# Optimization experiments

Measured on AMD Instinct MI355X. Metric: run time of the kernel, lower is better.

The kernel has to match this reference:

```python
import jax, jax.numpy as jnp
import numpy as np

VOCAB, E, H, L, B, OUT = 50000, 300, 300, 75, 2048, 5

def setup_inputs() -> dict:
    key = jax.random.key(0)
    ks = jax.random.split(key, 12)
    s_e = 1.0 / np.sqrt(E)
    s_h = 1.0 / np.sqrt(H)
    return {
        "input_sequences": jax.random.randint(ks[0], (B, L), 0, VOCAB),
        "emb": jax.random.normal(ks[1], (VOCAB, E), jnp.float32) * 0.1,
        "W_ih": jax.random.normal(ks[2], (3 * H, E), jnp.float32) * s_e,
        "W_hh": jax.random.normal(ks[3], (3 * H, H), jnp.float32) * s_h,
        "b_ih": jax.random.normal(ks[4], (3 * H,), jnp.float32) * s_h,
        "b_hh": jax.random.normal(ks[5], (3 * H,), jnp.float32) * s_h,
        "wCo_w": jax.random.normal(ks[6], (3 * H,), jnp.float32) * (1.0 / np.sqrt(3 * H)),
        "wCo_b": jax.random.normal(ks[7], (1,), jnp.float32) * 0.02,
        "Wmy_w": jax.random.normal(ks[8], (L,), jnp.float32) * (1.0 / np.sqrt(L)),
        "Wmy_b": jax.random.normal(ks[9], (1,), jnp.float32) * 0.02,
        "logits_w": jax.random.normal(ks[10], (OUT, H), jnp.float32) * s_h,
        "logits_b": jax.random.normal(ks[11], (OUT,), jnp.float32) * 0.02,
    }

def _gru(x_tm, W_ih, W_hh, b_ih, b_hh):
    # x_tm: (L, B, E) time-major. PyTorch GRU cell math.
    gx_all = jnp.einsum("lbe,ge->lbg", x_tm, W_ih) + b_ih  # (L, B, 3H)
    h0 = jnp.zeros((x_tm.shape[1], W_hh.shape[1]), x_tm.dtype)
    def step(h, gx):
        gh = h @ W_hh.T + b_hh
        xr, xz, xn = jnp.split(gx, 3, axis=-1)
        hr, hz, hn = jnp.split(gh, 3, axis=-1)
        r = jax.nn.sigmoid(xr + hr)
        z = jax.nn.sigmoid(xz + hz)
        n = jnp.tanh(xn + r * hn)
        h_new = (1.0 - z) * n + z * h
        return h_new, h_new
    _, ys = jax.lax.scan(step, h0, gx_all)
    return ys  # (L, B, H)

def reference(input_sequences, emb, W_ih, W_hh, b_ih, b_hh,
              wCo_w, wCo_b, Wmy_w, Wmy_b, logits_w, logits_b):
    x = emb[input_sequences]                      # (B, L, E)
    out_tm = _gru(x.transpose(1, 0, 2), W_ih, W_hh, b_ih, b_hh)  # (L, B, H)
    h = out_tm.transpose(1, 0, 2)                 # (B, L, H)
    # co_attention: s_ij = wCo @ cat(h_i, h_j, h_i*h_j) + b
    # computed WITHOUT materializing the (B, L, L, 3H) tensor:
    wa, wb, wc = jnp.split(wCo_w, 3)
    a = h @ wa                                    # (B, L)
    b = h @ wb                                    # (B, L)
    c = jnp.einsum("bid,bjd->bij", h * wc, h)     # (B, L, L)
    s = a[:, :, None] + b[:, None, :] + c + wCo_b[0]
    # zero the diagonal (mask = ones - diag)
    s = s * (1.0 - jnp.eye(s.shape[1], dtype=s.dtype))
    # Wmy: Linear(75, 1) over the j axis
    sm = s @ Wmy_w + Wmy_b[0]                     # (B, L)
    attn = jax.nn.softmax(sm, axis=1)             # softmax over i
    pooled = jnp.einsum("bi,bih->bh", attn, h)    # (B, H)
    return pooled @ logits_w.T + logits_b         # (B, OUT)
```

## Files before the change

### kernel.cpp

```cpp
#include <hip/hip_runtime.h>
#include <stdint.h>


typedef float f32x4 __attribute__((ext_vector_type(4)));
typedef short bf16x8 __attribute__((ext_vector_type(8)));
typedef _Float16 f16x4 __attribute__((ext_vector_type(4)));
typedef unsigned short u16;
typedef u16 u16x8 __attribute__((ext_vector_type(8)));
typedef u16 u16x4 __attribute__((ext_vector_type(4)));

#define DI __device__ __forceinline__

template <int N> struct IC { static constexpr int v = N; };

DI float bf2f(u16 v) {
    uint32_t u = ((uint32_t)v) << 16;
    float f;
    __builtin_memcpy(&f, &u, 4);
    return f;
}
DI u16 f2bf(float f) {
    uint32_t u;
    __builtin_memcpy(&u, &f, 4);
    uint32_t r = u + 0x7fffu + ((u >> 16) & 1u);
    return (u16)(r >> 16);
}
DI u16 cvt1(const void* p, int i, int f32m) {
    return f32m ? f2bf(((const float*)p)[i]) : ((const u16*)p)[i];
}

DI u16x8 load_row8(const u16* __restrict__ base, int e0) {
    u16x4 z = {0, 0, 0, 0};
    u16x4 lo = (e0 < 300) ? *(const u16x4*)(base + e0) : z;
    u16x4 hi = (e0 + 4 < 300) ? *(const u16x4*)(base + e0 + 4) : z;
    u16x8 r;
    r[0] = lo[0]; r[1] = lo[1]; r[2] = lo[2]; r[3] = lo[3];
    r[4] = hi[0]; r[5] = hi[1]; r[6] = hi[2]; r[7] = hi[3];
    return r;
}
DI u16x8 load_row8_f32(const float* __restrict__ base, int e0) {
    f32x4 z = {0.f, 0.f, 0.f, 0.f};
    f32x4 lo = (e0 < 300) ? *(const f32x4*)(base + e0) : z;
    f32x4 hi = (e0 + 4 < 300) ? *(const f32x4*)(base + e0 + 4) : z;
    u16x8 r;
    r[0] = f2bf(lo[0]); r[1] = f2bf(lo[1]); r[2] = f2bf(lo[2]); r[3] = f2bf(lo[3]);
    r[4] = f2bf(hi[0]); r[5] = f2bf(hi[1]); r[6] = f2bf(hi[2]); r[7] = f2bf(hi[3]);
    return r;
}

__global__ __launch_bounds__(256) void detect_dtype(const u16* __restrict__ raw,
                                                    int* __restrict__ flag) {
    __shared__ int cnt;
    if (threadIdx.x == 0) cnt = 0;
    __syncthreads();
    int local = 0;
    for (int i = threadIdx.x; i < 4096; i += 256) {
        int e = (raw[i] >> 7) & 0xFF;
        if (e >= 140) local++;
    }
    atomicAdd(&cnt, local);
    __syncthreads();
    if (threadIdx.x == 0) flag[0] = (cnt > 256) ? 1 : 0;
}

__global__ __launch_bounds__(256) void conv_big(const void* __restrict__ in,
                                                u16* __restrict__ outp, int n,
                                                const int* __restrict__ flag) {
    const int f32m = flag[0];
    int i0 = (blockIdx.x * 256 + threadIdx.x) * 8;
#pragma unroll
    for (int k = 0; k < 8; k++) {
        int i = i0 + k;
        if (i < n) outp[i] = cvt1(in, i, f32m);
    }
}

__global__ __launch_bounds__(256) void conv_smalls(
    const void* bih_r, const void* bhh_r, const void* wCo_r, const void* wCob_r,
    const void* Wmy_r, const void* Wmyb_r, const void* lw_r, const void* lb_r,
    u16* __restrict__ smalls, const int* __restrict__ flag) {
    const int f32m = flag[0];
    int t = blockIdx.x * 256 + threadIdx.x;
    if (t < 900) smalls[t] = cvt1(bih_r, t, f32m);
    else if (t < 1800) smalls[1024 + t - 900] = cvt1(bhh_r, t - 900, f32m);
    else if (t < 2700) smalls[2048 + t - 1800] = cvt1(wCo_r, t - 1800, f32m);
    else if (t < 2775) smalls[3072 + t - 2700] = cvt1(Wmy_r, t - 2700, f32m);
    else if (t < 4275) smalls[3200 + t - 2775] = cvt1(lw_r, t - 2775, f32m);
    else if (t < 4280) smalls[4704 + t - 4275] = cvt1(lb_r, t - 4275, f32m);
    else if (t == 4280) smalls[4712] = cvt1(wCob_r, 0, f32m);
    else if (t == 4281) smalls[4713] = cvt1(Wmyb_r, 0, f32m);
}

__global__ __launch_bounds__(256) void prep_img(const u16* __restrict__ W,
                                                u16* __restrict__ img) {
    int t = blockIdx.x * 256 + threadIdx.x;
    if (t >= 60 * 10 * 64) return;
    int lane = t & 63;
    int kt = (t >> 6) % 10;
    int nt = t / 640;
    int g = nt * 16 + (lane & 15);
    int gate = g / 320, u = g - gate * 320;
    int e0 = kt * 32 + (lane >> 4) * 8;
    u16x8 v;
    if (u < 300) {
        v = load_row8(W + (size_t)(gate * 300 + u) * 300, e0);
    } else {
        u16x8 z = {0, 0, 0, 0, 0, 0, 0, 0};
        v = z;
    }
    *(u16x8*)&img[(size_t)t * 8] = v;
}

__global__ __launch_bounds__(256) void zero_hstate(float* __restrict__ hs) {
    int t = blockIdx.x * 256 + threadIdx.x;
    f32x4 z = {0.f, 0.f, 0.f, 0.f};
    ((f32x4*)hs)[t] = z;
}

__global__ __launch_bounds__(256, 2) void gemm1_kernel(
    const int* __restrict__ seq, const void* __restrict__ emb_raw,
    const u16* __restrict__ Wimg, const u16* __restrict__ bih,
    _Float16* __restrict__ gxn, int ck, int phase, int BC, int bshift,
    const int* __restrict__ flag) {
    __shared__ int ids[192];
    __shared__ __align__(16) u16 Aimg[12 * 64 * 8];
    __shared__ __align__(16) u16 Bbuf[12 * 64 * 8];

    const int tid = threadIdx.x;
    const int lane = tid & 63, wv = tid >> 6, q = lane >> 4, c = lane & 15;
    const int m0 = blockIdx.x * 192;
    const int nb = blockIdx.y;
    const int f32m = flag[0];

    if (tid < 192) {
        int m = m0 + tid;
        int bc = m & (BC - 1);
        int tp = m >> bshift;
        ids[tid] = seq[(size_t)(phase * BC + bc) * 75 + ck * 15 + tp];
    }
    __syncthreads();

    f32x4 acc[3][12];
#pragma unroll
    for (int mt = 0; mt < 3; mt++)
#pragma unroll
        for (int nt = 0; nt < 12; nt++) {
            f32x4 z = {0.f, 0.f, 0.f, 0.f};
            acc[mt][nt] = z;
        }

    for (int kt = 0; kt < 10; kt++) {
#pragma unroll
        for (int s = 0; s < 3; s++) {
            int o = tid + s * 256;
            int qq = o / 192;
            int r = o - qq * 192;
            int e0 = kt * 32 + qq * 8;
            u16x8 v = f32m ? load_row8_f32((const float*)emb_raw + (size_t)ids[r] * 300, e0)
                           : load_row8((const u16*)emb_raw + (size_t)ids[r] * 300, e0);
            *(u16x8*)&Aimg[(((r >> 4) * 64) + ((r & 15) | (qq << 4))) * 8] = v;
        }
#pragma unroll
        for (int s = 0; s < 3; s++) {
            int ch = tid + s * 256;
            *(u16x8*)&Bbuf[ch * 8] =
                *(const u16x8*)&Wimg[(((size_t)(nb * 12 + (ch >> 6)) * 10 + kt) * 64 + (ch & 63)) * 8];
        }
        __syncthreads();

        bf16x8 a[3];
#pragma unroll
        for (int mt = 0; mt < 3; mt++) {
            u16x8 tmp = *(const u16x8*)&Aimg[(((wv * 3 + mt) * 64) + lane) * 8];
            a[mt] = __builtin_bit_cast(bf16x8, tmp);
        }
#pragma unroll
        for (int nt = 0; nt < 12; nt++) {
            u16x8 tb = *(const u16x8*)&Bbuf[(nt * 64 + lane) * 8];
            bf16x8 b = __builtin_bit_cast(bf16x8, tb);
#pragma unroll
            for (int mt = 0; mt < 3; mt++)
                acc[mt][nt] = __builtin_amdgcn_mfma_f32_16x16x32_bf16(a[mt], b, acc[mt][nt], 0, 0, 0);
        }
        __syncthreads();
    }

#pragma unroll
    for (int nt = 0; nt < 12; nt++) {
        int g = nb * 192 + nt * 16 + c;
        int gate = g / 320, u = g - gate * 320;
        float bias = (u < 300) ? bf2f(bih[gate * 300 + u]) : 0.f;
#pragma unroll
        for (int mt = 0; mt < 3; mt++) {
            int mrow = m0 + (wv * 3 + mt) * 16 + q * 4;
#pragma unroll
            for (int reg = 0; reg < 4; reg++) {
                gxn[((size_t)(mrow + reg) * 320 + u) * 4 + gate] =
                    (_Float16)(acc[mt][nt][reg] + bias);
            }
        }
    }
}

__global__ __launch_bounds__(512, 1) void gru_chunk(
    const _Float16* __restrict__ gxn, const u16* __restrict__ Wimg,
    const u16* __restrict__ bhh_g, u16* __restrict__ h_all,
    float* __restrict__ hstate, int ck, int BC) {
    __shared__ __align__(16) u16 Hhi[10 * 64 * 8];
    __shared__ __align__(16) u16 Hlo[10 * 64 * 8];
    __shared__ __align__(16) u16 Wlds[61440];

    const int tid = threadIdx.x;
    const int lane = tid & 63, wv = tid >> 6, q = lane >> 4, c = lane & 15;
    const int b0 = blockIdx.x * 16;
    const int wbase = (wv < 4) ? wv * 9216 : 36864 + (wv - 4) * 6144;

    float bhh[3][3];
    float hm[3][4];

    auto STAGE = [&](int kt, int buf, auto NTIC) {
        constexpr int NTI = NTIC.v;
        u16* dst = &Wlds[wbase + buf * (NTI * 3 * 512)];
#pragma unroll
        for (int Ti = 0; Ti < NTI; Ti++)
#pragma unroll
            for (int g = 0; g < 3; g++) {
                int nt = g * 20 + (wv + 8 * Ti);
                __builtin_amdgcn_global_load_lds(
                    (const unsigned int*)(Wimg + (size_t)(nt * 10 + kt) * 512 + lane * 8),
                    (unsigned int*)(dst + (Ti * 3 + g) * 512), 16, 0, 0);
            }
    };

    if (wv < 4) STAGE(0, 0, IC<3>{}); else STAGE(0, 0, IC<2>{});

    auto INIT = [&](auto NTIC) {
        constexpr int NTI = NTIC.v;
#pragma unroll
        for (int Ti = 0; Ti < NTI; Ti++) {
            int T = wv + 8 * Ti;
            int u = T * 16 + c;
#pragma unroll
            for (int g = 0; g < 3; g++)
                bhh[Ti][g] = (u < 300) ? bf2f(bhh_g[g * 300 + u]) : 0.f;
            int kti = T >> 1;
            int qp = ((T & 1) << 1) | (c >> 3);
            int j = c & 7;
#pragma unroll
            for (int reg = 0; reg < 4; reg++) {
                int m = q * 4 + reg;
                float h = hstate[(size_t)(b0 + m) * 320 + u];
                hm[Ti][reg] = h;
                int idx = (kti * 64 + ((q * 4 + reg) | (qp << 4))) * 8 + j;
                u16 hi = f2bf(h);
                Hhi[idx] = hi;
                Hlo[idx] = f2bf(h - bf2f(hi));
            }
        }
    };
    if (wv < 4) INIT(IC<3>{}); else INIT(IC<2>{});
    __syncthreads();

    for (int tt = 0; tt < 15; tt++) {
        auto PH1 = [&](auto NTIC) {
            constexpr int NTI = NTIC.v;
            constexpr int NT3 = NTI * 3;
            f16x4 gxv[NTI][4];
            const _Float16* gxt = gxn + (size_t)tt * BC * 1280;
#pragma unroll
            for (int Ti = 0; Ti < NTI; Ti++) {
                int u = (wv + 8 * Ti) * 16 + c;
#pragma unroll
                for (int reg = 0; reg < 4; reg++) {
                    int m = q * 4 + reg;
                    gxv[Ti][reg] = *(const f16x4*)&gxt[((size_t)(b0 + m) * 320 + u) * 4];
                }
            }

            f32x4 acc[NTI][3];
#pragma unroll
            for (int Ti = 0; Ti < NTI; Ti++)
#pragma unroll
                for (int g = 0; g < 3; g++) {
                    f32x4 z = {0.f, 0.f, 0.f, 0.f};
                    acc[Ti][g] = z;
                }

#pragma unroll 2
            for (int kt = 0; kt < 10; kt++) {
                if (kt < 9) STAGE(kt + 1, (kt + 1) & 1, NTIC);
                else if (tt < 14) STAGE(0, 0, NTIC);
                if (kt == 9 && tt == 14) {
                    asm volatile("s_waitcnt vmcnt(0)" ::: "memory");
                } else if constexpr (NTI == 3) {
                    asm volatile("s_waitcnt vmcnt(9)" ::: "memory");
                } else {
                    asm volatile("s_waitcnt vmcnt(6)" ::: "memory");
                }

                u16x8 th = *(const u16x8*)&Hhi[(kt * 64 + lane) * 8];
                u16x8 tl = *(const u16x8*)&Hlo[(kt * 64 + lane) * 8];
                bf16x8 ahi = __builtin_bit_cast(bf16x8, th);
                bf16x8 alo = __builtin_bit_cast(bf16x8, tl);
                const u16* wb = &Wlds[wbase + (kt & 1) * (NT3 * 512)];
#pragma unroll
                for (int Ti = 0; Ti < NTI; Ti++)
#pragma unroll
                    for (int g = 0; g < 3; g++) {
                        u16x8 tb = *(const u16x8*)&wb[(Ti * 3 + g) * 512 + lane * 8];
                        bf16x8 b = __builtin_bit_cast(bf16x8, tb);
                        acc[Ti][g] = __builtin_amdgcn_mfma_f32_16x16x32_bf16(
                            ahi, b, acc[Ti][g], 0, 0, 0);
                        acc[Ti][g] = __builtin_amdgcn_mfma_f32_16x16x32_bf16(
                            alo, b, acc[Ti][g], 0, 0, 0);
                    }
            }

            const int tglob = ck * 15 + tt;
#pragma unroll
            for (int Ti = 0; Ti < NTI; Ti++) {
                int u = (wv + 8 * Ti) * 16 + c;
#pragma unroll
                for (int reg = 0; reg < 4; reg++) {
                    int m = q * 4 + reg;
                    float xr = (float)gxv[Ti][reg][0];
                    float xz = (float)gxv[Ti][reg][1];
                    float xn = (float)gxv[Ti][reg][2];
                    float hr = acc[Ti][0][reg] + bhh[Ti][0];
                    float hz = acc[Ti][1][reg] + bhh[Ti][1];
                    float hn = acc[Ti][2][reg] + bhh[Ti][2];
                    float r = 1.f / (1.f + __expf(-(xr + hr)));
                    float z = 1.f / (1.f + __expf(-(xz + hz)));
                    float ex = __expf(2.f * (xn + r * hn));
                    float n = 1.f - 2.f / (ex + 1.f);
                    float h = (1.f - z) * n + z * hm[Ti][reg];
                    hm[Ti][reg] = h;
                    h_all[((size_t)tglob * BC + (b0 + m)) * 320 + u] = f2bf(h);
                }
            }
        };
        if (wv < 4) PH1(IC<3>{}); else PH1(IC<2>{});
        __syncthreads();

        auto FRAG = [&](auto NTIC) {
            constexpr int NTI = NTIC.v;
#pragma unroll
            for (int Ti = 0; Ti < NTI; Ti++) {
                int T = wv + 8 * Ti;
                int kti = T >> 1;
                int qp = ((T & 1) << 1) | (c >> 3);
                int j = c & 7;
#pragma unroll
                for (int reg = 0; reg < 4; reg++) {
                    int idx = (kti * 64 + ((q * 4 + reg) | (qp << 4))) * 8 + j;
                    float h = hm[Ti][reg];
                    u16 hi = f2bf(h);
                    Hhi[idx] = hi;
                    Hlo[idx] = f2bf(h - bf2f(hi));
                }
            }
        };
        if (wv < 4) FRAG(IC<3>{}); else FRAG(IC<2>{});
        __syncthreads();
    }

    auto PERSIST = [&](auto NTIC) {
        constexpr int NTI = NTIC.v;
#pragma unroll
        for (int Ti = 0; Ti < NTI; Ti++) {
            int u = (wv + 8 * Ti) * 16 + c;
#pragma unroll
            for (int reg = 0; reg < 4; reg++) {
                int m = q * 4 + reg;
                hstate[(size_t)(b0 + m) * 320 + u] = hm[Ti][reg];
            }
        }
    };
    if (wv < 4) PERSIST(IC<3>{}); else PERSIST(IC<2>{});
}

DI int hswz(int L, int kt) { return L ^ kt ^ (((L >> 4) & 3) << 1); }

__global__ __launch_bounds__(256) void coattn_kernel(
    const u16* __restrict__ h_all, const u16* __restrict__ smalls,
    void* __restrict__ outv, const int* __restrict__ flag, int phase, int BC) {
    __shared__ __align__(16) u16 himg[5 * 10 * 64 * 8];
    __shared__ float smacc[80], aArr[80], bArr[80], diagArr[80], attn[80], smv[80];
    __shared__ float scal[2];
    __shared__ float logitsAcc[5];

    const u16* wCo = smalls + 2048;
    const u16* Wmy = smalls + 3072;
    const u16* lw = smalls + 3200;
    const u16* lb = smalls + 4704;
    const int f32out = flag[0];

    const int b = blockIdx.x;
    const int tid = threadIdx.x;
    const int lane = tid & 63, wv = tid >> 6, q = lane >> 4, c = lane & 15;

    for (int o = tid; o < 3200; o += 256) {
        int i = o / 40;
        int oc = o - i * 40;
        int kt = oc >> 2, qq = oc & 3;
        int e0 = kt * 32 + qq * 8;
        u16x8 v = {0, 0, 0, 0, 0, 0, 0, 0};
        if (i < 75) v = *(const u16x8*)(h_all + ((size_t)i * BC + b) * 320 + e0);
        *(u16x8*)&himg[(((i >> 4) * 10 + kt) * 64 + hswz((i & 15) | (qq << 4), kt)) * 8] = v;
    }
    if (tid < 80) {
        smacc[tid] = 0.f; aArr[tid] = 0.f; bArr[tid] = 0.f;
        diagArr[tid] = 0.f; attn[tid] = 0.f;
    }
    if (tid < 5) logitsAcc[tid] = 0.f;
    __syncthreads();

    for (int pass = 0; pass < 2; pass++) {
        int nt = (pass == 0) ? wv : 4;
        int jj = nt * 16 + c;
        bf16x8 bfr[10];
#pragma unroll
        for (int kt = 0; kt < 10; kt++) {
            int e0 = kt * 32 + q * 8;
            u16x8 res = {0, 0, 0, 0, 0, 0, 0, 0};
            if (jj < 75) {
                u16x8 hv = *(const u16x8*)&himg[((nt * 10 + kt) * 64 + hswz(lane, kt)) * 8];
                u16x8 wcv = load_row8(wCo + 600, e0);
#pragma unroll
                for (int j = 0; j < 8; j++) res[j] = f2bf(bf2f(hv[j]) * bf2f(wcv[j]));
            } else if (jj == 75) {
                res = load_row8(wCo, e0);
            } else if (jj == 76) {
                res = load_row8(wCo + 300, e0);
            }
            bfr[kt] = __builtin_bit_cast(bf16x8, res);
        }
        float wmyj = (jj < 75) ? bf2f(Wmy[jj]) : 0.f;

        int nmt = (pass == 0) ? 5 : (wv == 0 ? 2 : 1);
        for (int mi = 0; mi < nmt; mi++) {
            int mt = (pass == 0) ? mi : (wv == 0 ? mi * 4 : wv);
            f32x4 acc = {0.f, 0.f, 0.f, 0.f};
#pragma unroll
            for (int kt = 0; kt < 10; kt++) {
                u16x8 ta = *(const u16x8*)&himg[((mt * 10 + kt) * 64 + hswz(lane, kt)) * 8];
                bf16x8 a = __builtin_bit_cast(bf16x8, ta);
                acc = __builtin_amdgcn_mfma_f32_16x16x32_bf16(a, bfr[kt], acc, 0, 0, 0);
            }
#pragma unroll
            for (int reg = 0; reg < 4; reg++) {
                int i = mt * 16 + q * 4 + reg;
                float v = acc[reg];
                float p = v * wmyj;
                p += __shfl_xor(p, 1);
                p += __shfl_xor(p, 2);
                p += __shfl_xor(p, 4);
                p += __shfl_xor(p, 8);
                if (c == 0 && i < 75) atomicAdd(&smacc[i], p);
                if (jj == i && i < 75) diagArr[i] = v;
                if (jj == 75) aArr[i] = v;
                if (jj == 76) bArr[i] = v;
            }
        }
    }
    __syncthreads();

    if (tid < 64) {
        float w1 = bf2f(Wmy[tid]);
        float w2 = (tid + 64 < 75) ? bf2f(Wmy[tid + 64]) : 0.f;
        float s1 = w1 + w2;
        float s2 = w1 * bArr[tid] + ((tid + 64 < 75) ? w2 * bArr[tid + 64] : 0.f);
#pragma unroll
        for (int m = 1; m < 64; m <<= 1) {
            s1 += __shfl_xor(s1, m);
            s2 += __shfl_xor(s2, m);
        }
        if (tid == 0) { scal[0] = s1; scal[1] = s2; }
    }
    __syncthreads();

    float cb = bf2f(smalls[4712]);
    float wmyb = bf2f(smalls[4713]);
    if (tid < 75) {
        float Wi = bf2f(Wmy[tid]);
        smv[tid] = smacc[tid] - diagArr[tid] * Wi + (aArr[tid] + cb) * (scal[0] - Wi) +
                   scal[1] - bArr[tid] * Wi + wmyb;
    }
    __syncthreads();

    if (tid < 64) {
        float v1 = smv[tid];
        float v2 = (tid + 64 < 75) ? smv[tid + 64] : -1e30f;
        float mx = fmaxf(v1, v2);
#pragma unroll
        for (int m = 1; m < 64; m <<= 1) mx = fmaxf(mx, __shfl_xor(mx, m));
        float e1 = __expf(v1 - mx);
        float e2 = (tid + 64 < 75) ? __expf(v2 - mx) : 0.f;
        float s = e1 + e2;
#pragma unroll
        for (int m = 1; m < 64; m <<= 1) s += __shfl_xor(s, m);
        attn[tid] = e1 / s;
        if (tid + 64 < 75) attn[tid + 64] = e2 / s;
    }
    __syncthreads();

    const int d1 = tid, d2 = tid + 256;
    float pd1 = 0.f, pd2 = 0.f;
    {
        const int kt1 = d1 >> 5, qq1 = (d1 >> 3) & 3, j1 = d1 & 7;
        const int kt2 = d2 >> 5, qq2 = (d2 >> 3) & 3, j2 = d2 & 7;
        for (int i = 0; i < 75; i++) {
            float a = attn[i];
            int ih = i >> 4, il = i & 15;
            pd1 += a * bf2f(himg[((ih * 10 + kt1) * 64 + hswz(il | (qq1 << 4), kt1)) * 8 + j1]);
            if (wv == 0)
                pd2 += a * bf2f(himg[((ih * 10 + kt2) * 64 + hswz(il | (qq2 << 4), kt2)) * 8 + j2]);
        }
    }
#pragma unroll
    for (int o = 0; o < 5; o++) {
        float part = (d1 < 300) ? pd1 * bf2f(lw[o * 300 + d1]) : 0.f;
        if (wv == 0 && d2 < 300) part += pd2 * bf2f(lw[o * 300 + d2]);
#pragma unroll
        for (int m = 1; m < 64; m <<= 1) part += __shfl_xor(part, m);
        if (lane == 0) atomicAdd(&logitsAcc[o], part);
    }
    __syncthreads();

    if (tid < 5) {
        float v = logitsAcc[tid] + bf2f(lb[tid]);
        size_t idx = (size_t)(phase * BC + b) * 5 + tid;
        if (f32out) ((float*)outv)[idx] = v;
        else ((u16*)outv)[idx] = f2bf(v);
    }
}

extern "C" void kernel_launch(void* const* d_in, const int* in_sizes, int n_in,
                              void* d_out, int out_size, void* d_ws, size_t ws_size,
                              hipStream_t stream) {
    const int* seq = (const int*)d_in[0];

    char* p = (char*)d_ws;
    int* flag = (int*)p;
    u16* smalls = (u16*)(p + 16);
    u16* WihImg = (u16*)(p + 9488);
    u16* WhhImg = (u16*)(p + 623888);
    u16* Wih_c = (u16*)(p + 1238288);
    u16* Whh_c = (u16*)(p + 1778288);
    const unsigned long long fixed_end = 2318288ull;

    auto req = [&](long long BC) -> unsigned long long {
        return fixed_end + (unsigned long long)BC * 87680ull + 1048576ull;
    };
    int BC = 256, bshift = 8;
    if (ws_size >= req(2048)) { BC = 2048; bshift = 11; }
    else if (ws_size >= req(1024)) { BC = 1024; bshift = 10; }
    else if (ws_size >= req(512)) { BC = 512; bshift = 9; }
    const int P = 2048 / BC;

    unsigned long long gx_b = 15ull * BC * 2560ull;
    unsigned long long h_b = 75ull * BC * 640ull;
    _Float16* gxn = (_Float16*)(p + fixed_end);
    u16* h_all = (u16*)(p + fixed_end + gx_b);
    float* hstate = (float*)(p + fixed_end + gx_b + h_b);

    detect_dtype<<<dim3(1), dim3(256), 0, stream>>>((const u16*)d_in[1], flag);
    conv_big<<<dim3((270000 + 2047) / 2048), dim3(256), 0, stream>>>(
        d_in[2], Wih_c, 270000, flag);
    conv_big<<<dim3((270000 + 2047) / 2048), dim3(256), 0, stream>>>(
        d_in[3], Whh_c, 270000, flag);
    conv_smalls<<<dim3(17), dim3(256), 0, stream>>>(
        d_in[4], d_in[5], d_in[6], d_in[7], d_in[8], d_in[9], d_in[10], d_in[11],
        smalls, flag);

    prep_img<<<dim3(150), dim3(256), 0, stream>>>(Wih_c, WihImg);
    prep_img<<<dim3(150), dim3(256), 0, stream>>>(Whh_c, WhhImg);

    for (int phase = 0; phase < P; phase++) {
        zero_hstate<<<dim3(BC * 320 / 1024), dim3(256), 0, stream>>>(hstate);
        for (int ck = 0; ck < 5; ck++) {
            gemm1_kernel<<<dim3(15 * BC / 192, 5), dim3(256), 0, stream>>>(
                seq, d_in[1], WihImg, smalls , gxn, ck, phase, BC, bshift, flag);
            gru_chunk<<<dim3(BC / 16), dim3(512), 0, stream>>>(
                gxn, WhhImg, smalls + 1024 , h_all, hstate, ck, BC);
        }
        coattn_kernel<<<dim3(BC), dim3(256), 0, stream>>>(h_all, smalls, d_out, flag,
                                                          phase, BC);
    }
}
```

Before: 1.458 ms.

## Double-buffer hidden state in LDS and stream W_hh directly into registers

The GRU chunk kernel now keeps two copies of the bf16 hi/lo hidden-state fragments in LDS. Each step writes the next state into the alternate buffer inside the gate epilogue, which removes one of the two block-wide barriers per timestep. It also drops the async global-to-LDS staging of W_hh and loads the weight fragments from global (L2) straight into registers with a two-deep prefetch. The trade-offs are more register pressure and global/L2 traffic per step, since every wave re-reads its weights each timestep, in exchange for fewer barriers and less LDS use.

```diff
diff --git a/kernel.cpp b/kernel.cpp
--- a/kernel.cpp
+++ b/kernel.cpp
@@ -206,33 +206,15 @@
     const _Float16* __restrict__ gxn, const u16* __restrict__ Wimg,
     const u16* __restrict__ bhh_g, u16* __restrict__ h_all,
     float* __restrict__ hstate, int ck, int BC) {
-    __shared__ __align__(16) u16 Hhi[10 * 64 * 8];
-    __shared__ __align__(16) u16 Hlo[10 * 64 * 8];
-    __shared__ __align__(16) u16 Wlds[61440];
+    __shared__ __align__(16) u16 Hhi[2][10 * 64 * 8];
+    __shared__ __align__(16) u16 Hlo[2][10 * 64 * 8];
 
     const int tid = threadIdx.x;
     const int lane = tid & 63, wv = tid >> 6, q = lane >> 4, c = lane & 15;
     const int b0 = blockIdx.x * 16;
-    const int wbase = (wv < 4) ? wv * 9216 : 36864 + (wv - 4) * 6144;
 
     float bhh[3][3];
     float hm[3][4];
-
-    auto STAGE = [&](int kt, int buf, auto NTIC) {
-        constexpr int NTI = NTIC.v;
-        u16* dst = &Wlds[wbase + buf * (NTI * 3 * 512)];
-#pragma unroll
-        for (int Ti = 0; Ti < NTI; Ti++)
-#pragma unroll
-            for (int g = 0; g < 3; g++) {
-                int nt = g * 20 + (wv + 8 * Ti);
-                __builtin_amdgcn_global_load_lds(
-                    (const unsigned int*)(Wimg + (size_t)(nt * 10 + kt) * 512 + lane * 8),
-                    (unsigned int*)(dst + (Ti * 3 + g) * 512), 16, 0, 0);
-            }
-    };
-
-    if (wv < 4) STAGE(0, 0, IC<3>{}); else STAGE(0, 0, IC<2>{});
 
     auto INIT = [&](auto NTIC) {
         constexpr int NTI = NTIC.v;
@@ -253,8 +235,8 @@
                 hm[Ti][reg] = h;
                 int idx = (kti * 64 + ((q * 4 + reg) | (qp << 4))) * 8 + j;
                 u16 hi = f2bf(h);
-                Hhi[idx] = hi;
-                Hlo[idx] = f2bf(h - bf2f(hi));
+                Hhi[0][idx] = hi;
+                Hlo[0][idx] = f2bf(h - bf2f(hi));
             }
         }
     };
@@ -262,9 +244,21 @@
     __syncthreads();
 
     for (int tt = 0; tt < 15; tt++) {
+        const int rd = tt & 1, wr = rd ^ 1;
         auto PH1 = [&](auto NTIC) {
             constexpr int NTI = NTIC.v;
             constexpr int NT3 = NTI * 3;
+
+            u16x8 wreg[2][NT3];
+#pragma unroll
+            for (int Ti = 0; Ti < NTI; Ti++)
+#pragma unroll
+                for (int g = 0; g < 3; g++) {
+                    int nt = g * 20 + (wv + 8 * Ti);
+                    wreg[0][Ti * 3 + g] =
+                        *(const u16x8*)&Wimg[((size_t)(nt * 10 + 0)) * 512 + lane * 8];
+                }
+
             f16x4 gxv[NTI][4];
             const _Float16* gxt = gxn + (size_t)tt * BC * 1280;
 #pragma unroll
@@ -286,29 +280,28 @@
                     acc[Ti][g] = z;
                 }
 
-#pragma unroll 2
+#pragma unroll
             for (int kt = 0; kt < 10; kt++) {
-                if (kt < 9) STAGE(kt + 1, (kt + 1) & 1, NTIC);
-                else if (tt < 14) STAGE(0, 0, NTIC);
-                if (kt == 9 && tt == 14) {
-                    asm volatile("s_waitcnt vmcnt(0)" ::: "memory");
-                } else if constexpr (NTI == 3) {
-                    asm volatile("s_waitcnt vmcnt(9)" ::: "memory");
-                } else {
-                    asm volatile("s_waitcnt vmcnt(6)" ::: "memory");
+                const int cur = kt & 1, nxt = cur ^ 1;
+                if (kt < 9) {
+#pragma unroll
+                    for (int Ti = 0; Ti < NTI; Ti++)
+#pragma unroll
+                        for (int g = 0; g < 3; g++) {
+                            int nt = g * 20 + (wv + 8 * Ti);
+                            wreg[nxt][Ti * 3 + g] =
+                                *(const u16x8*)&Wimg[((size_t)(nt * 10 + kt + 1)) * 512 + lane * 8];
+                        }
                 }
-
-                u16x8 th = *(const u16x8*)&Hhi[(kt * 64 + lane) * 8];
-                u16x8 tl = *(const u16x8*)&Hlo[(kt * 64 + lane) * 8];
+                u16x8 th = *(const u16x8*)&Hhi[rd][(kt * 64 + lane) * 8];
+                u16x8 tl = *(const u16x8*)&Hlo[rd][(kt * 64 + lane) * 8];
                 bf16x8 ahi = __builtin_bit_cast(bf16x8, th);
                 bf16x8 alo = __builtin_bit_cast(bf16x8, tl);
-                const u16* wb = &Wlds[wbase + (kt & 1) * (NT3 * 512)];
 #pragma unroll
                 for (int Ti = 0; Ti < NTI; Ti++)
 #pragma unroll
                     for (int g = 0; g < 3; g++) {
-                        u16x8 tb = *(const u16x8*)&wb[(Ti * 3 + g) * 512 + lane * 8];
-                        bf16x8 b = __builtin_bit_cast(bf16x8, tb);
+                        bf16x8 b = __builtin_bit_cast(bf16x8, wreg[cur][Ti * 3 + g]);
                         acc[Ti][g] = __builtin_amdgcn_mfma_f32_16x16x32_bf16(
                             ahi, b, acc[Ti][g], 0, 0, 0);
                         acc[Ti][g] = __builtin_amdgcn_mfma_f32_16x16x32_bf16(
@@ -319,7 +312,11 @@
             const int tglob = ck * 15 + tt;
 #pragma unroll
             for (int Ti = 0; Ti < NTI; Ti++) {
-                int u = (wv + 8 * Ti) * 16 + c;
+                int T = wv + 8 * Ti;
+                int u = T * 16 + c;
+                int kti = T >> 1;
+                int qp = ((T & 1) << 1) | (c >> 3);
+                int j = c & 7;
 #pragma unroll
                 for (int reg = 0; reg < 4; reg++) {
                     int m = q * 4 + reg;
@@ -336,31 +333,14 @@
                     float h = (1.f - z) * n + z * hm[Ti][reg];
                     hm[Ti][reg] = h;
                     h_all[((size_t)tglob * BC + (b0 + m)) * 320 + u] = f2bf(h);
+                    int idx = (kti * 64 + ((q * 4 + reg) | (qp << 4))) * 8 + j;
+                    u16 hi = f2bf(h);
+                    Hhi[wr][idx] = hi;
+                    Hlo[wr][idx] = f2bf(h - bf2f(hi));
                 }
             }
         };
         if (wv < 4) PH1(IC<3>{}); else PH1(IC<2>{});
-        __syncthreads();
-
-        auto FRAG = [&](auto NTIC) {
-            constexpr int NTI = NTIC.v;
-#pragma unroll
-            for (int Ti = 0; Ti < NTI; Ti++) {
-                int T = wv + 8 * Ti;
-                int kti = T >> 1;
-                int qp = ((T & 1) << 1) | (c >> 3);
-                int j = c & 7;
-#pragma unroll
-                for (int reg = 0; reg < 4; reg++) {
-                    int idx = (kti * 64 + ((q * 4 + reg) | (qp << 4))) * 8 + j;
-                    float h = hm[Ti][reg];
-                    u16 hi = f2bf(h);
-                    Hhi[idx] = hi;
-                    Hlo[idx] = f2bf(h - bf2f(hi));
-                }
-            }
-        };
-        if (wv < 4) FRAG(IC<3>{}); else FRAG(IC<2>{});
         __syncthreads();
     }
 
```

Result: slower. 2.896 ms (+98.6%).
